# Kernel optimization log

Measured on AMD Instinct MI355X. Metric: run time of the kernel, lower is better.

## Reference

```python
import jax, jax.numpy as jnp
import numpy as np

B, S, V, E, H, EMB = 512, 400, 50000, 512, 256, 128


def setup_inputs() -> dict:
    key = jax.random.key(0)
    ks = jax.random.split(key, 20)
    f = lambda i, shape, s=1.0: jax.random.normal(ks[i], shape, jnp.float32) * s
    return dict(
        coverage=jax.random.uniform(ks[0], (B, S), jnp.float32),
        enc_out=f(1, (B, S, E)),
        h0=f(2, (B, H)),
        c0=f(3, (B, H)),
        attn=jax.nn.softmax(f(4, (B, S)), axis=1),
        dec_input=jax.random.randint(ks[5], (B, 1), 0, V),
        enc_inputs=jax.random.randint(ks[6], (B, S), 0, V),
        emb_table=f(7, (V, EMB), 0.02),
        W_ih=f(8, (4 * H, EMB + E), 0.05),
        W_hh=f(9, (4 * H, H), 0.05),
        b_ih=jnp.zeros(4 * H, jnp.float32),
        b_hh=jnp.zeros(4 * H, jnp.float32),
        awh_W=f(10, (H, E), 0.05),
        awh_b=jnp.zeros(H, jnp.float32),
        aws_W=f(11, (H, H), 0.05),
        aws_b=jnp.zeros(H, jnp.float32),
        awc=jax.random.uniform(ks[12], (H,), jnp.float32),
        av=jax.random.uniform(ks[13], (H,), jnp.float32),
        wh=jax.random.uniform(ks[14], (E,), jnp.float32),
        ws=jax.random.uniform(ks[15], (H,), jnp.float32),
        wx=jax.random.uniform(ks[16], (EMB,), jnp.float32),
        v_W=f(17, (V, H), 0.05),
        v_b=jnp.zeros(V, jnp.float32),
    )


def reference(coverage, enc_out, h0, c0, attn, dec_input, enc_inputs,
              emb_table, W_ih, W_hh, b_ih, b_hh,
              awh_W, awh_b, aws_W, aws_b, awc, av,
              wh, ws, wx, v_W, v_b):
    b, s, e = enc_out.shape
    vocab = emb_table.shape[0]

    # context = bmm(attn[B,1,S], enc_out[B,S,E]) -> [B,1,E]
    context = jnp.einsum('bs,bse->be', attn, enc_out)  # [B,E]
    embed = emb_table[dec_input[:, 0]]                 # [B,EMB]
    x = jnp.concatenate([context, embed], axis=1)      # [B,E+EMB]

    # LSTMCell (torch gate order: i, f, g, o)
    gates = x @ W_ih.T + b_ih + h0 @ W_hh.T + b_hh     # [B,4H]
    i, f_, g, o = jnp.split(gates, 4, axis=1)
    c_t = jax.nn.sigmoid(f_) * c0 + jax.nn.sigmoid(i) * jnp.tanh(g)
    h_t = jax.nn.sigmoid(o) * jnp.tanh(c_t)

    p_vocab = jax.nn.softmax(h_t @ v_W.T + v_b, axis=1)  # [B,V]
    p_gen = jax.nn.sigmoid(context @ wh + h_t @ ws + embed @ wx)[:, None]  # [B,1]

    # Bahdanau attention with coverage
    wh_app = jnp.einsum('bse,he->bsh', enc_out, awh_W) + awh_b  # [B,S,H]
    ws_app = (h_t @ aws_W.T + aws_b)[:, None, :]                # [B,1,H]
    wc_app = coverage[:, :, None] * awc                         # [B,S,H]
    energy = jnp.tanh(wh_app + ws_app + wc_app) @ av            # [B,S]
    new_attn = jax.nn.softmax(energy, axis=1)

    coverage_loss = jnp.sum(jnp.minimum(new_attn, coverage))
    new_coverage = coverage + new_attn

    attn_scores = jnp.zeros((b, vocab), p_vocab.dtype).at[jnp.arange(b)[:, None], enc_inputs].set(new_attn)

    output = p_gen * p_vocab + (1.0 - p_gen) * attn_scores
    return output, new_coverage, (h_t, c_t), new_attn, coverage_loss
```

## Files before the change

kernel.cpp:

```cpp
#include <hip/hip_runtime.h>
#include <math.h>

#define Bd   512
#define Sd   400
#define Vd   50000
#define Ed   512
#define Hd   256
#define EMBd 128
#define XHs  896
#define Gd   1024

#define OFF_COV  25600000
#define OFF_H    25804800
#define OFF_C    25935872
#define OFF_ATTN 26066944
#define OFF_LOSS 26271744

#define WS_XH     0
#define WS_GATES  458752
#define WS_WSAPP  983040
#define WS_PGEN   1114112
#define WS_ENERGY 1114624
#define WS_LOSSB  1319424
#define WS_RMAX   1319936
#define WS_RSCALE 1320448

typedef __attribute__((ext_vector_type(8))) short short8;
typedef __attribute__((ext_vector_type(4))) float f32x4;

__device__ __forceinline__ float sigmoid_f(float x){ return 1.f/(1.f + __expf(-x)); }
__device__ __forceinline__ float tanh_f(float x){ return 1.f - 2.f/(__expf(2.f*x) + 1.f); }

__device__ __forceinline__ void gload_lds16(const void* g, void* l){
  __builtin_amdgcn_global_load_lds((const __attribute__((address_space(1))) void*)g,
                                   (__attribute__((address_space(3))) void*)l, 16, 0, 0);
}

__global__ __launch_bounds__(256) void k_context(
    const float* __restrict__ attn, const float* __restrict__ enc_out,
    const float* __restrict__ h0, const int* __restrict__ dec_input,
    const float* __restrict__ emb_table, float* __restrict__ xh)
{
  int b = blockIdx.x, t = threadIdx.x;
  __shared__ float sa[Sd];
  for (int s = t; s < Sd; s += 256) sa[s] = attn[(size_t)b*Sd + s];
  __syncthreads();
  const float* ep = enc_out + (size_t)b*Sd*Ed;
  float acc0 = 0.f, acc1 = 0.f;
  #pragma unroll 4
  for (int s = 0; s < Sd; ++s){
    float a = sa[s];
    acc0 += a * ep[(size_t)s*Ed + t];
    acc1 += a * ep[(size_t)s*Ed + t + 256];
  }
  float* xrow = xh + (size_t)b*XHs;
  xrow[t]       = acc0;
  xrow[t + 256] = acc1;
  if (t < EMBd){
    int tok = dec_input[b];
    xrow[Ed + t] = emb_table[(size_t)tok*EMBd + t];
  }
  xrow[Ed + EMBd + t] = h0[(size_t)b*Hd + t];
}

__global__ __launch_bounds__(256) void k_gates(
    const float* __restrict__ xh, const float* __restrict__ W_ih,
    const float* __restrict__ W_hh, const float* __restrict__ b_ih,
    const float* __restrict__ b_hh, float* __restrict__ gates)
{
  __shared__ float Al[32*36];
  __shared__ float Wl[64*33];
  int tid = threadIdx.x;
  int col0 = blockIdx.x * 64;
  int row0 = blockIdx.y * 32;
  int cg = tid & 15, rg = tid >> 4;
  float acc[2][4] = {{0,0,0,0},{0,0,0,0}};
  int alr = tid >> 3, alk = (tid & 7) * 4;
  int wlj = tid >> 2, wlk = (tid & 3) * 8;
  for (int kt = 0; kt < 28; ++kt){
    int k0 = kt * 32;
    float4 a4 = *(const float4*)(xh + (size_t)(row0+alr)*XHs + k0 + alk);
    *(float4*)(Al + alr*36 + alk) = a4;
    {
      const float* src;
      if (k0 < Ed + EMBd) src = W_ih + (size_t)(col0+wlj)*(Ed+EMBd) + k0 + wlk;
      else                src = W_hh + (size_t)(col0+wlj)*Hd + (k0 - (Ed+EMBd)) + wlk;
      #pragma unroll
      for (int q = 0; q < 8; ++q) Wl[wlj*33 + wlk + q] = src[q];
    }
    __syncthreads();
    #pragma unroll 4
    for (int k = 0; k < 32; ++k){
      float a0 = Al[(rg*2+0)*36 + k];
      float a1 = Al[(rg*2+1)*36 + k];
      #pragma unroll
      for (int j = 0; j < 4; ++j){
        float w = Wl[(cg + 16*j)*33 + k];
        acc[0][j] += a0 * w;
        acc[1][j] += a1 * w;
      }
    }
    __syncthreads();
  }
  #pragma unroll
  for (int i = 0; i < 2; ++i){
    int row = row0 + rg*2 + i;
    #pragma unroll
    for (int j = 0; j < 4; ++j){
      int col = col0 + cg + 16*j;
      gates[(size_t)row*Gd + col] = acc[i][j] + b_ih[col] + b_hh[col];
    }
  }
}

__global__ __launch_bounds__(256) void k_lstm(
    const float* __restrict__ gates, const float* __restrict__ c0,
    float* __restrict__ dout)
{
  int idx = blockIdx.x*256 + threadIdx.x;
  int b = idx >> 8, h = idx & 255;
  const float* g = gates + (size_t)b*Gd;
  float xi = g[h], xf = g[Hd + h], xg = g[2*Hd + h], xo = g[3*Hd + h];
  float c  = sigmoid_f(xf)*c0[idx] + sigmoid_f(xi)*tanh_f(xg);
  float ht = sigmoid_f(xo)*tanh_f(c);
  dout[OFF_C + idx] = c;
  dout[OFF_H + idx] = ht;
}

__global__ __launch_bounds__(256) void k_wcvt(
    const float* __restrict__ W, short* __restrict__ hi, short* __restrict__ lo)
{
  int i = blockIdx.x*256 + threadIdx.x;
  float4 w = ((const float4*)W)[i];
  float xs[4] = {w.x, w.y, w.z, w.w};
  short h4[4], l4[4];
  #pragma unroll
  for (int j = 0; j < 4; ++j){
    unsigned u = __float_as_uint(xs[j]);
    h4[j] = (short)(u >> 16);
    float hf = __uint_as_float(u & 0xffff0000u);
    l4[j] = (short)(__float_as_uint(xs[j] - hf) >> 16);
  }
  ((short4*)hi)[i] = make_short4(h4[0], h4[1], h4[2], h4[3]);
  ((short4*)lo)[i] = make_short4(l4[0], l4[1], l4[2], l4[3]);
}

__global__ __launch_bounds__(256) void k_wsapp(
    const float* __restrict__ ht, const float* __restrict__ aws_W,
    const float* __restrict__ aws_b, float* __restrict__ wsapp)
{
  int b = blockIdx.x, t = threadIdx.x;
  __shared__ float hrow[Hd];
  hrow[t] = ht[(size_t)b*Hd + t];
  __syncthreads();
  const float4* w4 = (const float4*)(aws_W + (size_t)t*Hd);
  float acc = 0.f;
  #pragma unroll 4
  for (int k4 = 0; k4 < Hd/4; ++k4){
    float4 w = w4[k4];
    int k = k4*4;
    acc += hrow[k]*w.x + hrow[k+1]*w.y + hrow[k+2]*w.z + hrow[k+3]*w.w;
  }
  wsapp[(size_t)b*Hd + t] = acc + aws_b[t];
}

__global__ __launch_bounds__(256) void k_pgen(
    const float* __restrict__ xh, const float* __restrict__ ht,
    const float* __restrict__ wh, const float* __restrict__ wsv,
    const float* __restrict__ wx, float* __restrict__ pgen)
{
  int b = blockIdx.x, t = threadIdx.x;
  __shared__ float red[256];
  const float* x = xh + (size_t)b*XHs;
  float part = x[t]*wh[t] + x[t+256]*wh[t+256];
  part += ht[(size_t)b*Hd + t] * wsv[t];
  if (t < EMBd) part += x[Ed + t] * wx[t];
  red[t] = part; __syncthreads();
  for (int off = 128; off > 0; off >>= 1){
    if (t < off) red[t] += red[t + off];
    __syncthreads();
  }
  if (t == 0) pgen[b] = sigmoid_f(red[0]);
}

__global__ __launch_bounds__(256) void k_energy_mfma(
    const float* __restrict__ enc_out, const short* __restrict__ Whi,
    const short* __restrict__ Wlo, const float* __restrict__ awh_b,
    const float* __restrict__ wsapp, const float* __restrict__ coverage,
    const float* __restrict__ awc, const float* __restrict__ av,
    float* __restrict__ energy)
{
  __shared__ short Ah[64*32], Alo[64*32];
  __shared__ short Bh[256*32], Blo[256*32];
  __shared__ float s_av[256], s_bias[256], s_awc[256];
  __shared__ float red[4][64];
  int tid = threadIdx.x;
  int wid = tid >> 6, lane = tid & 63;
  int row0 = blockIdx.x * 64;

  s_av[tid] = av[tid]; s_bias[tid] = awh_b[tid]; s_awc[tid] = awc[tid];

  f32x4 acc[4][4] = {};

  int ar = tid >> 2, as_ = tid & 3;
  int a_st = ar*32 + (as_ ^ ((ar>>1)&3))*8;
  const float* ag = enc_out + (size_t)(row0 + ar)*Ed + as_*8;

  int b_r[4], b_s[4];
  #pragma unroll
  for (int c = 0; c < 4; ++c){
    int ch = wid*4 + c;
    int r  = ch*16 + (lane>>2);
    b_r[c] = r;
    b_s[c] = (lane&3) ^ ((r>>1)&3);
  }

  int n0 = wid*64;
  int a_rd[4], b_rd[4];
  #pragma unroll
  for (int m = 0; m < 4; ++m){
    int r = m*16 + (lane&15);
    a_rd[m] = r*32 + (((lane>>4) ^ ((r>>1)&3)))*8;
  }
  #pragma unroll
  for (int n = 0; n < 4; ++n){
    int c = n0 + n*16 + (lane&15);
    b_rd[n] = c*32 + (((lane>>4) ^ ((c>>1)&3)))*8;
  }

  for (int kt = 0; kt < Ed/32; ++kt){
    int k0 = kt*32;
    #pragma unroll
    for (int c = 0; c < 4; ++c){
      int ch = wid*4 + c;
      const short* gh = Whi + (size_t)b_r[c]*Ed + k0 + b_s[c]*8;
      const short* gl = Wlo + (size_t)b_r[c]*Ed + k0 + b_s[c]*8;
      gload_lds16(gh, &Bh[ch*512]);
      gload_lds16(gl, &Blo[ch*512]);
    }
    float4 a0 = *(const float4*)(ag + k0);
    float4 a1 = *(const float4*)(ag + k0 + 4);
    float xs[8] = {a0.x,a0.y,a0.z,a0.w,a1.x,a1.y,a1.z,a1.w};
    short8 h8, l8;
    #pragma unroll
    for (int q = 0; q < 8; ++q){
      unsigned u = __float_as_uint(xs[q]);
      h8[q] = (short)(u >> 16);
      float hf = __uint_as_float(u & 0xffff0000u);
      l8[q] = (short)(__float_as_uint(xs[q] - hf) >> 16);
    }
    *(short8*)&Ah[a_st]  = h8;
    *(short8*)&Alo[a_st] = l8;
    __syncthreads();

    short8 ah[4], al[4], bh[4], bl[4];
    #pragma unroll
    for (int m = 0; m < 4; ++m){
      ah[m] = *(const short8*)&Ah[a_rd[m]];
      al[m] = *(const short8*)&Alo[a_rd[m]];
    }
    #pragma unroll
    for (int n = 0; n < 4; ++n){
      bh[n] = *(const short8*)&Bh[b_rd[n]];
      bl[n] = *(const short8*)&Blo[b_rd[n]];
    }
    #pragma unroll
    for (int m = 0; m < 4; ++m){
      #pragma unroll
      for (int n = 0; n < 4; ++n){
        acc[m][n] = __builtin_amdgcn_mfma_f32_16x16x32_bf16(ah[m], bh[n], acc[m][n], 0, 0, 0);
        acc[m][n] = __builtin_amdgcn_mfma_f32_16x16x32_bf16(ah[m], bl[n], acc[m][n], 0, 0, 0);
        acc[m][n] = __builtin_amdgcn_mfma_f32_16x16x32_bf16(al[m], bh[n], acc[m][n], 0, 0, 0);
      }
    }
    __syncthreads();
  }

  int b0 = row0 / Sd;
  int b1 = b0 + 1; if (b1 > Bd-1) b1 = Bd-1;
  int split = (b0 + 1) * Sd;
  float avv[4], bbv[4], wcv[4], wv0[4], wv1[4];
  #pragma unroll
  for (int n = 0; n < 4; ++n){
    int h = n0 + n*16 + (lane&15);
    avv[n] = s_av[h]; bbv[n] = s_bias[h]; wcv[n] = s_awc[h];
    wv0[n] = wsapp[(size_t)b0*Hd + h];
    wv1[n] = wsapp[(size_t)b1*Hd + h];
  }
  #pragma unroll
  for (int m = 0; m < 4; ++m){
    #pragma unroll
    for (int j = 0; j < 4; ++j){
      int rt = m*16 + ((lane>>4)<<2) + j;
      int grow = row0 + rt;
      bool hib = (grow >= split);
      float cov = coverage[grow];
      float part = 0.f;
      #pragma unroll
      for (int n = 0; n < 4; ++n){
        float x = acc[m][n][j] + bbv[n] + (hib ? wv1[n] : wv0[n]) + cov*wcv[n];
        part += avv[n]*tanh_f(x);
      }
      part += __shfl_xor(part, 1, 16);
      part += __shfl_xor(part, 2, 16);
      part += __shfl_xor(part, 4, 16);
      part += __shfl_xor(part, 8, 16);
      if ((lane & 15) == 0) red[wid][rt] = part;
    }
  }
  __syncthreads();
  if (tid < 64)
    energy[row0 + tid] = red[0][tid] + red[1][tid] + red[2][tid] + red[3][tid];
}

__global__ __launch_bounds__(256) void k_attn_softmax(
    const float* __restrict__ energy, const float* __restrict__ coverage,
    float* __restrict__ dout, float* __restrict__ loss_b)
{
  int b = blockIdx.x, t = threadIdx.x;
  __shared__ float red[256];
  const float* e = energy + (size_t)b*Sd;
  float e0 = e[t];
  float e1 = (t + 256 < Sd) ? e[t+256] : -1e30f;
  red[t] = fmaxf(e0, e1); __syncthreads();
  for (int off = 128; off > 0; off >>= 1){
    if (t < off) red[t] = fmaxf(red[t], red[t+off]);
    __syncthreads();
  }
  float m = red[0]; __syncthreads();
  float p0 = __expf(e0 - m);
  float p1 = (t + 256 < Sd) ? __expf(e1 - m) : 0.f;
  red[t] = p0 + p1; __syncthreads();
  for (int off = 128; off > 0; off >>= 1){
    if (t < off) red[t] += red[t+off];
    __syncthreads();
  }
  float inv = 1.f / red[0]; __syncthreads();
  float* attn_o = dout + OFF_ATTN + (size_t)b*Sd;
  float* cov_o  = dout + OFF_COV  + (size_t)b*Sd;
  float a0 = p0 * inv;
  float cv0 = coverage[(size_t)b*Sd + t];
  attn_o[t] = a0; cov_o[t] = cv0 + a0;
  float lp = fminf(a0, cv0);
  if (t + 256 < Sd){
    float a1 = p1 * inv;
    float cv1 = coverage[(size_t)b*Sd + t + 256];
    attn_o[t+256] = a1; cov_o[t+256] = cv1 + a1;
    lp += fminf(a1, cv1);
  }
  red[t] = lp; __syncthreads();
  for (int off = 128; off > 0; off >>= 1){
    if (t < off) red[t] += red[t+off];
    __syncthreads();
  }
  if (t == 0) loss_b[b] = red[0];
}

__global__ void k_loss(const float* __restrict__ loss_b, float* __restrict__ dout)
{
  __shared__ float red[256];
  int t = threadIdx.x;
  red[t] = loss_b[t] + loss_b[t + 256];
  __syncthreads();
  for (int off = 128; off > 0; off >>= 1){
    if (t < off) red[t] += red[t+off];
    __syncthreads();
  }
  if (t == 0) dout[OFF_LOSS] = red[0];
}

__global__ __launch_bounds__(256) void k_logits(
    const float* __restrict__ ht, const float* __restrict__ v_W,
    const float* __restrict__ v_b, float* __restrict__ out)
{
  __shared__ float Al[32*68];
  __shared__ float Wl[32*258];
  int tid = threadIdx.x;
  int col0 = blockIdx.x * 256;
  int row0 = blockIdx.y * 64;
  int cg = tid & 31, rg = tid >> 5;
  float acc[8][8];
  #pragma unroll
  for (int i=0;i<8;++i){
    #pragma unroll
    for (int j=0;j<8;++j) acc[i][j]=0.f;
  }
  int alr = tid >> 2, alk = (tid & 3) * 8;
  int wlh = tid >> 3, wlk = (tid & 7) * 4;
  for (int kt = 0; kt < Hd/32; ++kt){
    int k0 = kt * 32;
    const float* ap = ht + (size_t)(row0 + alr)*Hd + k0 + alk;
    float4 x0 = *(const float4*)ap;
    float4 x1 = *(const float4*)(ap + 4);
    Al[(alk+0)*68 + alr] = x0.x; Al[(alk+1)*68 + alr] = x0.y;
    Al[(alk+2)*68 + alr] = x0.z; Al[(alk+3)*68 + alr] = x0.w;
    Al[(alk+4)*68 + alr] = x1.x; Al[(alk+5)*68 + alr] = x1.y;
    Al[(alk+6)*68 + alr] = x1.z; Al[(alk+7)*68 + alr] = x1.w;
    #pragma unroll
    for (int p = 0; p < 8; ++p){
      int h = wlh + 32*p;
      int v = col0 + h; if (v > Vd-1) v = Vd-1;
      float4 w4 = *(const float4*)(v_W + (size_t)v*Hd + k0 + wlk);
      Wl[(wlk+0)*258 + h] = w4.x; Wl[(wlk+1)*258 + h] = w4.y;
      Wl[(wlk+2)*258 + h] = w4.z; Wl[(wlk+3)*258 + h] = w4.w;
    }
    __syncthreads();
    #pragma unroll 4
    for (int k = 0; k < 32; ++k){
      float a[8], w[8];
      *(float4*)(&a[0]) = *(const float4*)(Al + k*68 + rg*8);
      *(float4*)(&a[4]) = *(const float4*)(Al + k*68 + rg*8 + 4);
      #pragma unroll
      for (int j = 0; j < 4; ++j){
        float2 w2 = *(const float2*)(Wl + k*258 + cg*2 + 64*j);
        w[2*j] = w2.x; w[2*j+1] = w2.y;
      }
      #pragma unroll
      for (int i = 0; i < 8; ++i){
        #pragma unroll
        for (int j = 0; j < 8; ++j) acc[i][j] += a[i]*w[j];
      }
    }
    __syncthreads();
  }
  #pragma unroll
  for (int i = 0; i < 8; ++i){
    int row = row0 + rg*8 + i;
    float* orow = out + (size_t)row*Vd;
    #pragma unroll
    for (int j = 0; j < 4; ++j){
      int v0 = col0 + cg*2 + 64*j;
      if (v0 < Vd){
        float2 r;
        r.x = acc[i][2*j]   + v_b[v0];
        r.y = acc[i][2*j+1] + v_b[v0+1];
        *(float2*)(orow + v0) = r;
      }
    }
  }
}

__global__ __launch_bounds__(256) void k_vocab_stats(
    const float* __restrict__ logits, const float* __restrict__ pgen,
    float* __restrict__ rmax, float* __restrict__ rscale)
{
  int b = blockIdx.x, t = threadIdx.x;
  __shared__ float red[256];
  const float4* row = (const float4*)(logits + (size_t)b*Vd);
  float m = -1e30f;
  for (int i = t; i < Vd/4; i += 256){
    float4 x = row[i];
    m = fmaxf(m, fmaxf(fmaxf(x.x, x.y), fmaxf(x.z, x.w)));
  }
  red[t] = m; __syncthreads();
  for (int off = 128; off > 0; off >>= 1){
    if (t < off) red[t] = fmaxf(red[t], red[t+off]);
    __syncthreads();
  }
  m = red[0]; __syncthreads();
  float s = 0.f;
  for (int i = t; i < Vd/4; i += 256){
    float4 x = row[i];
    s += __expf(x.x-m) + __expf(x.y-m) + __expf(x.z-m) + __expf(x.w-m);
  }
  red[t] = s; __syncthreads();
  for (int off = 128; off > 0; off >>= 1){
    if (t < off) red[t] += red[t+off];
    __syncthreads();
  }
  if (t == 0){ rmax[b] = m; rscale[b] = pgen[b] / red[0]; }
}

__global__ __launch_bounds__(256) void k_vocab_norm(
    float* __restrict__ out, const float* __restrict__ rmax,
    const float* __restrict__ rscale)
{
  long long i4 = (long long)blockIdx.x*256 + threadIdx.x;
  int b = (int)(i4 / (Vd/4));
  float m = rmax[b], sc = rscale[b];
  float4* o = (float4*)out;
  float4 x = o[i4];
  x.x = sc*__expf(x.x - m); x.y = sc*__expf(x.y - m);
  x.z = sc*__expf(x.z - m); x.w = sc*__expf(x.w - m);
  o[i4] = x;
}

__global__ __launch_bounds__(256) void k_scatter(
    const int* __restrict__ enc_inputs, const float* __restrict__ pgen,
    float* __restrict__ dout)
{
  int idx = blockIdx.x*256 + threadIdx.x;
  int b = idx / Sd, s = idx - b*Sd;
  const int* row = enc_inputs + (size_t)b*Sd;
  int v = row[s];
  for (int s2 = s+1; s2 < Sd; ++s2) if (row[s2] == v) return;
  float pg = pgen[b];
  float a = dout[OFF_ATTN + idx];
  float* p = dout + (size_t)b*Vd + v;
  *p = *p + (1.f - pg)*a;
}

extern "C" void kernel_launch(void* const* d_in, const int* in_sizes, int n_in,
                              void* d_out, int out_size, void* d_ws, size_t ws_size,
                              hipStream_t stream)
{
  const float* coverage   = (const float*)d_in[0];
  const float* enc_out    = (const float*)d_in[1];
  const float* h0         = (const float*)d_in[2];
  const float* c0         = (const float*)d_in[3];
  const float* attn       = (const float*)d_in[4];
  const int*   dec_input  = (const int*)  d_in[5];
  const int*   enc_inputs = (const int*)  d_in[6];
  const float* emb_table  = (const float*)d_in[7];
  const float* W_ih       = (const float*)d_in[8];
  const float* W_hh       = (const float*)d_in[9];
  const float* b_ih       = (const float*)d_in[10];
  const float* b_hh       = (const float*)d_in[11];
  const float* awh_W      = (const float*)d_in[12];
  const float* awh_b      = (const float*)d_in[13];
  const float* aws_W      = (const float*)d_in[14];
  const float* aws_b      = (const float*)d_in[15];
  const float* awc        = (const float*)d_in[16];
  const float* av         = (const float*)d_in[17];
  const float* wh         = (const float*)d_in[18];
  const float* wsv        = (const float*)d_in[19];
  const float* wx         = (const float*)d_in[20];
  const float* v_W        = (const float*)d_in[21];
  const float* v_b        = (const float*)d_in[22];
  float* out = (float*)d_out;
  float* ws  = (float*)d_ws;

  float* xh     = ws + WS_XH;
  float* gates  = ws + WS_GATES;
  float* wsapp  = ws + WS_WSAPP;
  float* pgen   = ws + WS_PGEN;
  float* energy = ws + WS_ENERGY;
  float* loss_b = ws + WS_LOSSB;
  float* rmax   = ws + WS_RMAX;
  float* rscale = ws + WS_RSCALE;
  float* ht = out + OFF_H;

  short* Whi = (short*)gates;
  short* Wlo = Whi + 256*512;

  k_context<<<Bd, 256, 0, stream>>>(attn, enc_out, h0, dec_input, emb_table, xh);
  k_gates<<<dim3(Gd/64, Bd/32), 256, 0, stream>>>(xh, W_ih, W_hh, b_ih, b_hh, gates);
  k_lstm<<<(Bd*Hd)/256, 256, 0, stream>>>(gates, c0, out);
  k_wcvt<<<(Hd*Ed/4)/256, 256, 0, stream>>>(awh_W, Whi, Wlo);
  k_wsapp<<<Bd, 256, 0, stream>>>(ht, aws_W, aws_b, wsapp);
  k_pgen<<<Bd, 256, 0, stream>>>(xh, ht, wh, wsv, wx, pgen);
  k_energy_mfma<<<(Bd*Sd)/64, 256, 0, stream>>>(enc_out, Whi, Wlo, awh_b, wsapp, coverage, awc, av, energy);
  k_attn_softmax<<<Bd, 256, 0, stream>>>(energy, coverage, out, loss_b);
  k_loss<<<1, 256, 0, stream>>>(loss_b, out);
  k_logits<<<dim3((Vd + 255)/256, Bd/64), 256, 0, stream>>>(ht, v_W, v_b, out);
  k_vocab_stats<<<Bd, 256, 0, stream>>>(out, pgen, rmax, rscale);
  k_vocab_norm<<<(Bd*Vd/4)/256, 256, 0, stream>>>(out, rmax, rscale);
  k_scatter<<<(Bd*Sd)/256, 256, 0, stream>>>(enc_inputs, pgen, out);
}
```

Measured before the change: 1.271 ms.

## Compute vocab logits with bf16 MFMA and fuse wsapp/pgen kernels

The FP32 SIMT logits GEMM (512x50000x256) is replaced by a bf16 MFMA kernel. h_t is converted to bf16 inside the weight-convert kernel and v_W is rounded to bf16 on the fly while staging into LDS. The wsapp and pgen kernels are merged into one, and the energy kernel reuses LDS for its reduction and reads small vectors directly from global memory. This drops a costly FP32 GEMM and one launch, at the cost of single-bf16 rounding of logits with no hi/lo error compensation, which may hurt accuracy.

```diff
diff --git a/kernel.cpp b/kernel.cpp
--- a/kernel.cpp
+++ b/kernel.cpp
@@ -24,6 +24,7 @@
 #define WS_LOSSB  1319424
 #define WS_RMAX   1319936
 #define WS_RSCALE 1320448
+#define WS_HTBF   589824
 
 typedef __attribute__((ext_vector_type(8))) short short8;
 typedef __attribute__((ext_vector_type(4))) float f32x4;
@@ -128,30 +129,48 @@
 }
 
 __global__ __launch_bounds__(256) void k_wcvt(
-    const float* __restrict__ W, short* __restrict__ hi, short* __restrict__ lo)
-{
-  int i = blockIdx.x*256 + threadIdx.x;
-  float4 w = ((const float4*)W)[i];
-  float xs[4] = {w.x, w.y, w.z, w.w};
-  short h4[4], l4[4];
-  #pragma unroll
-  for (int j = 0; j < 4; ++j){
-    unsigned u = __float_as_uint(xs[j]);
-    h4[j] = (short)(u >> 16);
-    float hf = __uint_as_float(u & 0xffff0000u);
-    l4[j] = (short)(__float_as_uint(xs[j] - hf) >> 16);
-  }
-  ((short4*)hi)[i] = make_short4(h4[0], h4[1], h4[2], h4[3]);
-  ((short4*)lo)[i] = make_short4(l4[0], l4[1], l4[2], l4[3]);
-}
-
-__global__ __launch_bounds__(256) void k_wsapp(
+    const float* __restrict__ W, short* __restrict__ hi, short* __restrict__ lo,
+    const float* __restrict__ ht, short* __restrict__ htb)
+{
+  int bx = blockIdx.x;
+  if (bx < 128){
+    int i = bx*256 + threadIdx.x;
+    float4 w = ((const float4*)W)[i];
+    float xs[4] = {w.x, w.y, w.z, w.w};
+    short h4[4], l4[4];
+    #pragma unroll
+    for (int j = 0; j < 4; ++j){
+      unsigned u = __float_as_uint(xs[j]);
+      h4[j] = (short)(u >> 16);
+      float hf = __uint_as_float(u & 0xffff0000u);
+      l4[j] = (short)(__float_as_uint(xs[j] - hf) >> 16);
+    }
+    ((short4*)hi)[i] = make_short4(h4[0], h4[1], h4[2], h4[3]);
+    ((short4*)lo)[i] = make_short4(l4[0], l4[1], l4[2], l4[3]);
+  } else {
+    int i = (bx - 128)*256 + threadIdx.x;
+    float4 w = ((const float4*)ht)[i];
+    short h4[4];
+    h4[0] = (short)((__float_as_uint(w.x) + 0x8000u) >> 16);
+    h4[1] = (short)((__float_as_uint(w.y) + 0x8000u) >> 16);
+    h4[2] = (short)((__float_as_uint(w.z) + 0x8000u) >> 16);
+    h4[3] = (short)((__float_as_uint(w.w) + 0x8000u) >> 16);
+    ((short4*)htb)[i] = make_short4(h4[0], h4[1], h4[2], h4[3]);
+  }
+}
+
+__global__ __launch_bounds__(256) void k_post(
     const float* __restrict__ ht, const float* __restrict__ aws_W,
-    const float* __restrict__ aws_b, float* __restrict__ wsapp)
+    const float* __restrict__ aws_b, const float* __restrict__ xh,
+    const float* __restrict__ wh, const float* __restrict__ wsv,
+    const float* __restrict__ wx, float* __restrict__ wsapp,
+    float* __restrict__ pgen)
 {
   int b = blockIdx.x, t = threadIdx.x;
   __shared__ float hrow[Hd];
-  hrow[t] = ht[(size_t)b*Hd + t];
+  __shared__ float red[256];
+  float htv = ht[(size_t)b*Hd + t];
+  hrow[t] = htv;
   __syncthreads();
   const float4* w4 = (const float4*)(aws_W + (size_t)t*Hd);
   float acc = 0.f;
@@ -162,18 +181,9 @@
     acc += hrow[k]*w.x + hrow[k+1]*w.y + hrow[k+2]*w.z + hrow[k+3]*w.w;
   }
   wsapp[(size_t)b*Hd + t] = acc + aws_b[t];
-}
-
-__global__ __launch_bounds__(256) void k_pgen(
-    const float* __restrict__ xh, const float* __restrict__ ht,
-    const float* __restrict__ wh, const float* __restrict__ wsv,
-    const float* __restrict__ wx, float* __restrict__ pgen)
-{
-  int b = blockIdx.x, t = threadIdx.x;
-  __shared__ float red[256];
   const float* x = xh + (size_t)b*XHs;
   float part = x[t]*wh[t] + x[t+256]*wh[t+256];
-  part += ht[(size_t)b*Hd + t] * wsv[t];
+  part += htv * wsv[t];
   if (t < EMBd) part += x[Ed + t] * wx[t];
   red[t] = part; __syncthreads();
   for (int off = 128; off > 0; off >>= 1){
@@ -192,13 +202,9 @@
 {
   __shared__ short Ah[64*32], Alo[64*32];
   __shared__ short Bh[256*32], Blo[256*32];
-  __shared__ float s_av[256], s_bias[256], s_awc[256];
-  __shared__ float red[4][64];
   int tid = threadIdx.x;
   int wid = tid >> 6, lane = tid & 63;
   int row0 = blockIdx.x * 64;
-
-  s_av[tid] = av[tid]; s_bias[tid] = awh_b[tid]; s_awc[tid] = awc[tid];
 
   f32x4 acc[4][4] = {};
 
@@ -276,6 +282,7 @@
     __syncthreads();
   }
 
+  float* red = (float*)Bh;
   int b0 = row0 / Sd;
   int b1 = b0 + 1; if (b1 > Bd-1) b1 = Bd-1;
   int split = (b0 + 1) * Sd;
@@ -283,7 +290,7 @@
   #pragma unroll
   for (int n = 0; n < 4; ++n){
     int h = n0 + n*16 + (lane&15);
-    avv[n] = s_av[h]; bbv[n] = s_bias[h]; wcv[n] = s_awc[h];
+    avv[n] = av[h]; bbv[n] = awh_b[h]; wcv[n] = awc[h];
     wv0[n] = wsapp[(size_t)b0*Hd + h];
     wv1[n] = wsapp[(size_t)b1*Hd + h];
   }
@@ -305,12 +312,12 @@
       part += __shfl_xor(part, 2, 16);
       part += __shfl_xor(part, 4, 16);
       part += __shfl_xor(part, 8, 16);
-      if ((lane & 15) == 0) red[wid][rt] = part;
+      if ((lane & 15) == 0) red[wid*64 + rt] = part;
     }
   }
   __syncthreads();
   if (tid < 64)
-    energy[row0 + tid] = red[0][tid] + red[1][tid] + red[2][tid] + red[3][tid];
+    energy[row0 + tid] = red[tid] + red[64 + tid] + red[128 + tid] + red[192 + tid];
 }
 
 __global__ __launch_bounds__(256) void k_attn_softmax(
@@ -369,72 +376,93 @@
   if (t == 0) dout[OFF_LOSS] = red[0];
 }
 
-__global__ __launch_bounds__(256) void k_logits(
-    const float* __restrict__ ht, const float* __restrict__ v_W,
+__global__ __launch_bounds__(256) void k_logits_mfma(
+    const short* __restrict__ ht_bf, const float* __restrict__ v_W,
     const float* __restrict__ v_b, float* __restrict__ out)
 {
-  __shared__ float Al[32*68];
-  __shared__ float Wl[32*258];
+  __shared__ short Abf[128*32];
+  __shared__ short Bbf[256*32];
   int tid = threadIdx.x;
+  int wid = tid >> 6, lane = tid & 63;
   int col0 = blockIdx.x * 256;
-  int row0 = blockIdx.y * 64;
-  int cg = tid & 31, rg = tid >> 5;
-  float acc[8][8];
-  #pragma unroll
-  for (int i=0;i<8;++i){
-    #pragma unroll
-    for (int j=0;j<8;++j) acc[i][j]=0.f;
-  }
-  int alr = tid >> 2, alk = (tid & 3) * 8;
-  int wlh = tid >> 3, wlk = (tid & 7) * 4;
+  int row0 = blockIdx.y * 128;
+  int wr0 = (wid & 1) * 64, wc0 = (wid >> 1) * 128;
+
+  f32x4 acc[4][8] = {};
+
+  int ac_r[2], ac_s[2];
+  #pragma unroll
+  for (int c = 0; c < 2; ++c){
+    int ch = wid*2 + c;
+    int r = ch*16 + (lane >> 2);
+    ac_r[c] = r;
+    ac_s[c] = (lane & 3) ^ ((r >> 1) & 3);
+  }
+
+  int vrow = col0 + tid; if (vrow > Vd - 1) vrow = Vd - 1;
+  const float* bg = v_W + (size_t)vrow * Hd;
+  int bsw = (tid >> 1) & 3;
+
+  int a_rd[4], b_rd[8];
+  #pragma unroll
+  for (int m = 0; m < 4; ++m){
+    int r = wr0 + m*16 + (lane & 15);
+    a_rd[m] = r*32 + (((lane >> 4) ^ ((r >> 1) & 3)))*8;
+  }
+  #pragma unroll
+  for (int n = 0; n < 8; ++n){
+    int c = wc0 + n*16 + (lane & 15);
+    b_rd[n] = c*32 + (((lane >> 4) ^ ((c >> 1) & 3)))*8;
+  }
+
   for (int kt = 0; kt < Hd/32; ++kt){
     int k0 = kt * 32;
-    const float* ap = ht + (size_t)(row0 + alr)*Hd + k0 + alk;
-    float4 x0 = *(const float4*)ap;
-    float4 x1 = *(const float4*)(ap + 4);
-    Al[(alk+0)*68 + alr] = x0.x; Al[(alk+1)*68 + alr] = x0.y;
-    Al[(alk+2)*68 + alr] = x0.z; Al[(alk+3)*68 + alr] = x0.w;
-    Al[(alk+4)*68 + alr] = x1.x; Al[(alk+5)*68 + alr] = x1.y;
-    Al[(alk+6)*68 + alr] = x1.z; Al[(alk+7)*68 + alr] = x1.w;
-    #pragma unroll
-    for (int p = 0; p < 8; ++p){
-      int h = wlh + 32*p;
-      int v = col0 + h; if (v > Vd-1) v = Vd-1;
-      float4 w4 = *(const float4*)(v_W + (size_t)v*Hd + k0 + wlk);
-      Wl[(wlk+0)*258 + h] = w4.x; Wl[(wlk+1)*258 + h] = w4.y;
-      Wl[(wlk+2)*258 + h] = w4.z; Wl[(wlk+3)*258 + h] = w4.w;
-    }
-    __syncthreads();
-    #pragma unroll 4
-    for (int k = 0; k < 32; ++k){
-      float a[8], w[8];
-      *(float4*)(&a[0]) = *(const float4*)(Al + k*68 + rg*8);
-      *(float4*)(&a[4]) = *(const float4*)(Al + k*68 + rg*8 + 4);
+    #pragma unroll
+    for (int c = 0; c < 2; ++c){
+      const short* src = ht_bf + (size_t)(row0 + ac_r[c])*Hd + k0 + ac_s[c]*8;
+      gload_lds16(src, &Abf[(wid*2 + c)*512]);
+    }
+    unsigned p[16];
+    #pragma unroll
+    for (int q = 0; q < 8; ++q){
+      float4 f = *(const float4*)(bg + k0 + q*4);
+      unsigned u0 = __float_as_uint(f.x) + 0x8000u;
+      unsigned u1 = __float_as_uint(f.y) + 0x8000u;
+      unsigned u2 = __float_as_uint(f.z) + 0x8000u;
+      unsigned u3 = __float_as_uint(f.w) + 0x8000u;
+      p[q*2]   = (u1 & 0xffff0000u) | (u0 >> 16);
+      p[q*2+1] = (u3 & 0xffff0000u) | (u2 >> 16);
+    }
+    #pragma unroll
+    for (int s = 0; s < 4; ++s){
+      uint4 w4; w4.x = p[s*4]; w4.y = p[s*4+1]; w4.z = p[s*4+2]; w4.w = p[s*4+3];
+      *(uint4*)&Bbf[tid*32 + (s ^ bsw)*8] = w4;
+    }
+    __syncthreads();
+    short8 a[4];
+    #pragma unroll
+    for (int m = 0; m < 4; ++m) a[m] = *(const short8*)&Abf[a_rd[m]];
+    #pragma unroll
+    for (int n = 0; n < 8; ++n){
+      short8 bfr = *(const short8*)&Bbf[b_rd[n]];
       #pragma unroll
-      for (int j = 0; j < 4; ++j){
-        float2 w2 = *(const float2*)(Wl + k*258 + cg*2 + 64*j);
-        w[2*j] = w2.x; w[2*j+1] = w2.y;
-      }
+      for (int m = 0; m < 4; ++m)
+        acc[m][n] = __builtin_amdgcn_mfma_f32_16x16x32_bf16(a[m], bfr, acc[m][n], 0, 0, 0);
+    }
+    __syncthreads();
+  }
+
+  #pragma unroll
+  for (int n = 0; n < 8; ++n){
+    int col = col0 + wc0 + n*16 + (lane & 15);
+    if (col < Vd){
+      float bias = v_b[col];
       #pragma unroll
-      for (int i = 0; i < 8; ++i){
+      for (int m = 0; m < 4; ++m){
+        int rbase = row0 + wr0 + m*16 + ((lane >> 4) << 2);
         #pragma unroll
-        for (int j = 0; j < 8; ++j) acc[i][j] += a[i]*w[j];
-      }
-    }
-    __syncthreads();
-  }
-  #pragma unroll
-  for (int i = 0; i < 8; ++i){
-    int row = row0 + rg*8 + i;
-    float* orow = out + (size_t)row*Vd;
-    #pragma unroll
-    for (int j = 0; j < 4; ++j){
-      int v0 = col0 + cg*2 + 64*j;
-      if (v0 < Vd){
-        float2 r;
-        r.x = acc[i][2*j]   + v_b[v0];
-        r.y = acc[i][2*j+1] + v_b[v0+1];
-        *(float2*)(orow + v0) = r;
+        for (int j = 0; j < 4; ++j)
+          out[(size_t)(rbase + j)*Vd + col] = acc[m][n][j] + bias;
       }
     }
   }
@@ -540,19 +568,19 @@
   float* rscale = ws + WS_RSCALE;
   float* ht = out + OFF_H;
 
-  short* Whi = (short*)gates;
-  short* Wlo = Whi + 256*512;
+  short* Whi   = (short*)gates;
+  short* Wlo   = Whi + 256*512;
+  short* ht_bf = (short*)(ws + WS_HTBF);
 
   k_context<<<Bd, 256, 0, stream>>>(attn, enc_out, h0, dec_input, emb_table, xh);
   k_gates<<<dim3(Gd/64, Bd/32), 256, 0, stream>>>(xh, W_ih, W_hh, b_ih, b_hh, gates);
   k_lstm<<<(Bd*Hd)/256, 256, 0, stream>>>(gates, c0, out);
-  k_wcvt<<<(Hd*Ed/4)/256, 256, 0, stream>>>(awh_W, Whi, Wlo);
-  k_wsapp<<<Bd, 256, 0, stream>>>(ht, aws_W, aws_b, wsapp);
-  k_pgen<<<Bd, 256, 0, stream>>>(xh, ht, wh, wsv, wx, pgen);
+  k_wcvt<<<256, 256, 0, stream>>>(awh_W, Whi, Wlo, ht, ht_bf);
+  k_post<<<Bd, 256, 0, stream>>>(ht, aws_W, aws_b, xh, wh, wsv, wx, wsapp, pgen);
   k_energy_mfma<<<(Bd*Sd)/64, 256, 0, stream>>>(enc_out, Whi, Wlo, awh_b, wsapp, coverage, awc, av, energy);
   k_attn_softmax<<<Bd, 256, 0, stream>>>(energy, coverage, out, loss_b);
   k_loss<<<1, 256, 0, stream>>>(loss_b, out);
-  k_logits<<<dim3((Vd + 255)/256, Bd/64), 256, 0, stream>>>(ht, v_W, v_b, out);
+  k_logits_mfma<<<dim3((Vd + 255)/256, Bd/128), 256, 0, stream>>>(ht_bf, v_W, v_b, out);
   k_vocab_stats<<<Bd, 256, 0, stream>>>(out, pgen, rmax, rscale);
   k_vocab_norm<<<(Bd*Vd/4)/256, 256, 0, stream>>>(out, rmax, rscale);
   k_scatter<<<(Bd*Sd)/256, 256, 0, stream>>>(enc_inputs, pgen, out);
```

After: 1.161 ms. 8.7% less time.
